# Optimization experiments

Measured on AMD Instinct MI355X. Metric: run time of the kernel, lower is better.

## Reference

```python
import jax, jax.numpy as jnp
import numpy as np

N = 50000      # nodes
E = 800000     # edges (avg degree 16)
IN, HID, OUT = 128, 256, 64
G = 500        # graphs in the batch (100 nodes each)
NEG_SLOPE = 0.01
EPS = 1e-12


def setup_inputs() -> dict:
    key = jax.random.key(0)
    ks = jax.random.split(key, 9)
    x = jax.random.normal(ks[0], (N, IN), jnp.float32)
    edge_index = jax.random.randint(ks[1], (2, E), 0, N, dtype=jnp.int32)
    # sorted segment ids with every graph present (100 nodes per graph)
    batch = jnp.repeat(jnp.arange(G, dtype=jnp.int32), N // G)
    def lin(k, fan_in, fan_out):
        s = 1.0 / np.sqrt(fan_in)
        kw, kb = jax.random.split(k)
        W = jax.random.uniform(kw, (fan_in, fan_out), jnp.float32, -s, s)
        b = jax.random.uniform(kb, (fan_out,), jnp.float32, -s, s)
        return W, b
    W1, b1 = lin(ks[2], IN, HID)
    W2, b2 = lin(ks[3], HID, HID)
    W3, b3 = lin(ks[4], HID, OUT)
    return {"x": x, "edge_index": edge_index, "batch": batch,
            "W1": W1, "b1": b1, "W2": W2, "b2": b2, "W3": W3, "b3": b3}


def _sage_conv(x, edge_index, W, b):
    # SAGEConv(aggr='add', root_weight=False, normalize=True):
    # gather source features, scatter-add to targets, linear, L2 normalize.
    src, dst = edge_index[0], edge_index[1]
    agg = jax.ops.segment_sum(x[src], dst, num_segments=x.shape[0])  # [N, d_in]
    out = agg @ W + b                                                 # [N, d_out]
    nrm = jnp.linalg.norm(out, axis=-1, keepdims=True)
    return out / jnp.maximum(nrm, EPS)


def reference(x, edge_index, batch, W1, b1, W2, b2, W3, b3):
    h = _sage_conv(x, edge_index, W1, b1)
    h = jax.nn.leaky_relu(h, NEG_SLOPE)          # dropout p=0 -> identity
    h = _sage_conv(h, edge_index, W2, b2)
    h = jax.nn.leaky_relu(h, NEG_SLOPE)
    h = _sage_conv(h, edge_index, W3, b3)
    # get_zero_nodes: first node of each graph (batch sorted, all G present)
    mask = jnp.concatenate([jnp.ones((1,), bool), batch[1:] != batch[:-1]])
    first_idx = jnp.nonzero(mask, size=G)[0]
    return h[first_idx]                          # [G, OUT]
```

## Files before the change

### kernel.cpp

```cpp
#include <hip/hip_runtime.h>

#define N_NODES 50000
#define E_EDGES 800000
#define IN_DIM  128
#define HID_DIM 256
#define OUT_DIM 64
#define G_GRAPHS 500
#define CAP 64

typedef __attribute__((ext_vector_type(8))) short short8;
typedef __attribute__((ext_vector_type(4))) float float4v;

__device__ __forceinline__ float bf2f(unsigned short u) {
  union { unsigned int i; float f; } c; c.i = ((unsigned int)u) << 16; return c.f;
}
__device__ __forceinline__ unsigned short f2bf(float f) {
  union { float f; unsigned int i; } c; c.f = f;
  unsigned int x = c.i;
  x += 0x7FFFu + ((x >> 16) & 1u);
  return (unsigned short)(x >> 16);
}
__device__ __forceinline__ unsigned int fbits(float f) {
  union { float f; unsigned int i; } c; c.f = f; return c.i;
}
__device__ __forceinline__ float bits2f(unsigned int u) {
  union { unsigned int i; float f; } c; c.i = u; return c.f;
}


__global__ __launch_bounds__(256) void prep_build(
    const int* __restrict__ src, const int* __restrict__ dst,
    const int* __restrict__ batch,
    const float* __restrict__ x,
    const float* __restrict__ W1, const float* __restrict__ W2,
    int* __restrict__ deg, int* __restrict__ srcs, int* __restrict__ first_node,
    unsigned short* __restrict__ xb,
    unsigned short* __restrict__ W1t, unsigned short* __restrict__ W2t) {
  const int b = blockIdx.x, tid = threadIdx.x;
  if (b < 6250) {
    const int t = b * 256 + tid;
    const int i = t * 4;
    const float4 v = *(const float4*)(x + i);
    ushort4 u;
    u.x = f2bf(v.x); u.y = f2bf(v.y); u.z = f2bf(v.z); u.w = f2bf(v.w);
    *(ushort4*)(xb + i) = u;
    if (t < E_EDGES) {
      const int d = dst[t];
      const int pos = atomicAdd(&deg[d], 1);
      if (pos < CAP) srcs[(d << 6) + pos] = src[t];
    }
    if (t < N_NODES) {
      if (t == 0 || batch[t] != batch[t - 1]) first_node[batch[t]] = t;
    }
  } else {
    const int t = (b - 6250) * 256 + tid;
    if (t < 8192) {
      const int n = t >> 5, k0 = (t & 31) * 4;
      ushort4 o;
      o.x = f2bf(W1[(k0 + 0) * 256 + n]);
      o.y = f2bf(W1[(k0 + 1) * 256 + n]);
      o.z = f2bf(W1[(k0 + 2) * 256 + n]);
      o.w = f2bf(W1[(k0 + 3) * 256 + n]);
      *(ushort4*)&W1t[n * 128 + k0] = o;
    } else {
      const int v2 = t - 8192;
      const int n = v2 >> 6, k0 = (v2 & 63) * 4;
      ushort4 o;
      o.x = f2bf(W2[(k0 + 0) * 256 + n]);
      o.y = f2bf(W2[(k0 + 1) * 256 + n]);
      o.z = f2bf(W2[(k0 + 2) * 256 + n]);
      o.w = f2bf(W2[(k0 + 3) * 256 + n]);
      *(ushort4*)&W2t[n * 256 + k0] = o;
    }
  }
}


__global__ __launch_bounds__(64) void build_list2(
    const int* __restrict__ deg, const int* __restrict__ srcs,
    const int* __restrict__ first_node,
    unsigned char* __restrict__ need1, int* __restrict__ list2,
    int* __restrict__ cnt2) {
  const int g = blockIdx.x;
  const int lane = threadIdx.x;
  const int node = first_node[g];
  const int cnt = min(deg[node], CAP);
  int s = 0;
  if (lane < cnt) s = srcs[(node << 6) + lane];
  const unsigned long long m = __ballot(lane < cnt);
  int base = 0;
  if (lane == 0) base = atomicAdd(cnt2, __popcll(m));
  base = __shfl(base, 0);
  if (lane < cnt) {
    list2[base + lane] = s;
    const int c2 = min(deg[s], CAP);
    for (int q = 0; q < c2; ++q) need1[srcs[(s << 6) + q]] = 1;
  }
}

__global__ __launch_bounds__(256) void compact_list1(
    const unsigned char* __restrict__ need1,
    int* __restrict__ list1, int* __restrict__ cnt1) {
  __shared__ int wbase[4];
  const int tid = threadIdx.x;
  const int lane = tid & 63;
  const int wv = tid >> 6;
  const int i = blockIdx.x * 256 + tid;
  const bool f = (i < N_NODES) && need1[i];
  const unsigned long long m = __ballot(f);
  if (lane == 0) wbase[wv] = __popcll(m);
  __syncthreads();
  if (tid == 0) {
    const int t0 = wbase[0], t1 = wbase[1], t2 = wbase[2], t3 = wbase[3];
    const int b = atomicAdd(cnt1, t0 + t1 + t2 + t3);
    wbase[0] = b; wbase[1] = b + t0; wbase[2] = b + t0 + t1; wbase[3] = b + t0 + t1 + t2;
  }
  __syncthreads();
  if (f) list1[wbase[wv] + __popcll(m & ((1ull << lane) - 1ull))] = i;
}


template<int K>
__global__ __launch_bounds__(512, 8) void fused_layer(
    const unsigned short* __restrict__ H,
    const int* __restrict__ deg, const int* __restrict__ srcs,
    const unsigned short* __restrict__ Wt,
    const float* __restrict__ bias,
    unsigned short* __restrict__ Hout,
    const int* __restrict__ nodelist,
    const int* __restrict__ pcount)
{
  constexpr int M = 256;
  constexpr int TN = 16;
  constexpr int VPT = K / 64;
  constexpr int LDK = K + 8;
  __shared__ unsigned short a_hi[TN][LDK];
  __shared__ unsigned short a_lo[TN][LDK];
  __shared__ float ssq_tot[TN];
  __shared__ int nid_s[TN];
  const int tid = threadIdx.x;
  const int lane = tid & 63;
  const int wv = tid >> 6;

  const int total = __builtin_amdgcn_readfirstlane(*pcount);
  if (blockIdx.x * TN >= total) return;

  if (tid < TN) {
    int gi = blockIdx.x * TN + tid;
    if (gi >= total) gi = total - 1;
    nid_s[tid] = nodelist[gi];
    ssq_tot[tid] = 0.f;
  }
  __syncthreads();

  const unsigned short* hb = H + lane * VPT;
  const int node0 = __builtin_amdgcn_readfirstlane(nid_s[2 * wv]);
  const int node1 = __builtin_amdgcn_readfirstlane(nid_s[2 * wv + 1]);
  const int cnt0 = __builtin_amdgcn_readfirstlane(min(deg[node0], CAP));
  const int cnt1 = __builtin_amdgcn_readfirstlane(min(deg[node1], CAP));
  int idx0 = 0, idx1 = 0;
  if (lane < cnt0) idx0 = srcs[(node0 << 6) + lane];
  if (lane < cnt1) idx1 = srcs[(node1 << 6) + lane];

#pragma unroll
  for (int i = 0; i < 2; ++i) {
    const int nn = 2 * wv + i;
    const int cnt = i ? cnt1 : cnt0;
    const int idx = i ? idx1 : idx0;

    float acc[VPT];
#pragma unroll
    for (int j = 0; j < VPT; ++j) acc[j] = 0.f;

    int j = 0;
    for (; j + 16 <= cnt; j += 16) {
      int s[16];
#pragma unroll
      for (int u = 0; u < 16; ++u) s[u] = __builtin_amdgcn_readlane(idx, j + u);
      if constexpr (VPT == 4) {
        ushort4 r[16];
#pragma unroll
        for (int u = 0; u < 16; ++u) r[u] = *(const ushort4*)(hb + s[u] * K);
#pragma unroll
        for (int u = 0; u < 16; ++u) {
          acc[0] += bf2f(r[u].x); acc[1] += bf2f(r[u].y);
          acc[2] += bf2f(r[u].z); acc[3] += bf2f(r[u].w);
        }
      } else {
        ushort2 r[16];
#pragma unroll
        for (int u = 0; u < 16; ++u) r[u] = *(const ushort2*)(hb + s[u] * K);
#pragma unroll
        for (int u = 0; u < 16; ++u) {
          acc[0] += bf2f(r[u].x); acc[1] += bf2f(r[u].y);
        }
      }
    }
    for (; j < cnt; j += 8) {
      int s[8]; float w[8];
#pragma unroll
      for (int u = 0; u < 8; ++u) {
        const int q = j + u;
        const int qm = (q < cnt) ? q : (cnt - 1);
        s[u] = __builtin_amdgcn_readlane(idx, qm);
        w[u] = (q < cnt) ? 1.f : 0.f;
      }
      if constexpr (VPT == 4) {
        ushort4 r[8];
#pragma unroll
        for (int u = 0; u < 8; ++u) r[u] = *(const ushort4*)(hb + s[u] * K);
#pragma unroll
        for (int u = 0; u < 8; ++u) {
          acc[0] = fmaf(w[u], bf2f(r[u].x), acc[0]);
          acc[1] = fmaf(w[u], bf2f(r[u].y), acc[1]);
          acc[2] = fmaf(w[u], bf2f(r[u].z), acc[2]);
          acc[3] = fmaf(w[u], bf2f(r[u].w), acc[3]);
        }
      } else {
        ushort2 r[8];
#pragma unroll
        for (int u = 0; u < 8; ++u) r[u] = *(const ushort2*)(hb + s[u] * K);
#pragma unroll
        for (int u = 0; u < 8; ++u) {
          acc[0] = fmaf(w[u], bf2f(r[u].x), acc[0]);
          acc[1] = fmaf(w[u], bf2f(r[u].y), acc[1]);
        }
      }
    }

    unsigned short h[VPT], l[VPT];
#pragma unroll
    for (int jj = 0; jj < VPT; ++jj) {
      const unsigned int u = fbits(acc[jj]);
      h[jj] = (unsigned short)(u >> 16);
      const float res = acc[jj] - bits2f(u & 0xFFFF0000u);
      l[jj] = (unsigned short)(fbits(res) >> 16);
    }
    if constexpr (VPT == 4) {
      *(ushort4*)&a_hi[nn][lane * 4] = make_ushort4(h[0], h[1], h[2], h[3]);
      *(ushort4*)&a_lo[nn][lane * 4] = make_ushort4(l[0], l[1], l[2], l[3]);
    } else {
      *(ushort2*)&a_hi[nn][lane * 2] = make_ushort2(h[0], h[1]);
      *(ushort2*)&a_lo[nn][lane * 2] = make_ushort2(l[0], l[1]);
    }
  }
  __syncthreads();

  const int g = lane >> 4;
  const int lc = lane & 15;
  float4v dacc0 = (float4v){0.f, 0.f, 0.f, 0.f};
  float4v dacc1 = (float4v){0.f, 0.f, 0.f, 0.f};
  const unsigned short* W0 = Wt + (size_t)(wv * 16 + lc) * K + g * 8;
  const unsigned short* W1r = Wt + (size_t)((wv + 8) * 16 + lc) * K + g * 8;
#pragma unroll
  for (int ks = 0; ks < K / 32; ++ks) {
    const short8 ah = *(const short8*)&a_hi[lc][ks * 32 + g * 8];
    const short8 al = *(const short8*)&a_lo[lc][ks * 32 + g * 8];
    const short8 b0 = *(const short8*)(W0 + ks * 32);
    const short8 b1 = *(const short8*)(W1r + ks * 32);
    dacc0 = __builtin_amdgcn_mfma_f32_16x16x32_bf16(ah, b0, dacc0, 0, 0, 0);
    dacc0 = __builtin_amdgcn_mfma_f32_16x16x32_bf16(al, b0, dacc0, 0, 0, 0);
    dacc1 = __builtin_amdgcn_mfma_f32_16x16x32_bf16(ah, b1, dacc1, 0, 0, 0);
    dacc1 = __builtin_amdgcn_mfma_f32_16x16x32_bf16(al, b1, dacc1, 0, 0, 0);
  }

  const float bn0 = bias[wv * 16 + lc];
  const float bn1 = bias[(wv + 8) * 16 + lc];
  float4v o0 = dacc0 + bn0;
  float4v o1 = dacc1 + bn1;
  float sq[4];
#pragma unroll
  for (int r = 0; r < 4; ++r) sq[r] = o0[r] * o0[r] + o1[r] * o1[r];
#pragma unroll
  for (int off = 1; off < 16; off <<= 1) {
#pragma unroll
    for (int r = 0; r < 4; ++r) sq[r] += __shfl_xor(sq[r], off);
  }
  if (lc == 0) {
#pragma unroll
    for (int r = 0; r < 4; ++r) atomicAdd(&ssq_tot[g * 4 + r], sq[r]);
  }
  __syncthreads();

#pragma unroll
  for (int r = 0; r < 4; ++r) {
    const float inv = 1.f / fmaxf(sqrtf(ssq_tot[g * 4 + r]), 1e-12f);
    float v0 = o0[r] * inv;
    float v1 = o1[r] * inv;
    v0 = (v0 >= 0.f) ? v0 : 0.01f * v0;
    v1 = (v1 >= 0.f) ? v1 : 0.01f * v1;
    const int nd = nid_s[g * 4 + r];
    Hout[(size_t)nd * M + wv * 16 + lc] = f2bf(v0);
    Hout[(size_t)nd * M + (wv + 8) * 16 + lc] = f2bf(v1);
  }
}


__global__ __launch_bounds__(64) void layer3_kernel(
    const unsigned short* __restrict__ H2,
    const int* __restrict__ deg, const int* __restrict__ srcs,
    const int* __restrict__ first_node,
    const float* __restrict__ W,
    const float* __restrict__ bias,
    float* __restrict__ out)
{
  __shared__ float a_s[HID_DIM];
  const int g = blockIdx.x;
  const int lane = threadIdx.x;
  const int node = first_node[g];
  const int cnt = min(deg[node], CAP);
  float acc[4] = {0.f, 0.f, 0.f, 0.f};
  for (int p = 0; p < cnt; ++p) {
    const int s = srcs[(node << 6) + p];
    const ushort4 u = *(const ushort4*)(H2 + (size_t)s * HID_DIM + lane * 4);
    acc[0] += bf2f(u.x); acc[1] += bf2f(u.y); acc[2] += bf2f(u.z); acc[3] += bf2f(u.w);
  }
  *(float4*)&a_s[lane * 4] = make_float4(acc[0], acc[1], acc[2], acc[3]);
  __syncthreads();
  float o = bias[lane];
#pragma unroll 8
  for (int k = 0; k < HID_DIM; ++k) o += a_s[k] * W[k * OUT_DIM + lane];
  float ss = o * o;
#pragma unroll
  for (int off = 32; off > 0; off >>= 1) ss += __shfl_xor(ss, off);
  const float inv = 1.f / fmaxf(sqrtf(ss), 1e-12f);
  out[(size_t)g * OUT_DIM + lane] = o * inv;
}


extern "C" void kernel_launch(void* const* d_in, const int* in_sizes, int n_in,
                              void* d_out, int out_size, void* d_ws, size_t ws_size,
                              hipStream_t stream) {
  (void)in_sizes; (void)n_in; (void)out_size; (void)ws_size;
  const float* x   = (const float*)d_in[0];
  const int* ei    = (const int*)d_in[1];
  const int* batch = (const int*)d_in[2];
  const float* W1  = (const float*)d_in[3];
  const float* b1  = (const float*)d_in[4];
  const float* W2  = (const float*)d_in[5];
  const float* b2  = (const float*)d_in[6];
  const float* W3  = (const float*)d_in[7];
  const float* b3  = (const float*)d_in[8];
  const int* src = ei;
  const int* dst = ei + E_EDGES;

  char* ws = (char*)d_ws;
  size_t off = 0;
  auto alloc = [&](size_t bytes) {
    void* p = ws + off;
    off = (off + bytes + 255) & ~(size_t)255;
    return p;
  };
  int* deg    = (int*)alloc((size_t)N_NODES * 4);
  unsigned char* need1 = (unsigned char*)alloc((size_t)N_NODES);
  int* cnts   = (int*)alloc(256);
  const size_t zero_len = off;
  int* cnt1 = cnts;
  int* cnt2 = cnts + 1;

  int* srcs   = (int*)alloc((size_t)N_NODES * CAP * 4);
  int* first  = (int*)alloc((size_t)G_GRAPHS * 4);
  int* list1  = (int*)alloc((size_t)N_NODES * 4);
  int* list2  = (int*)alloc((size_t)G_GRAPHS * CAP * 4);
  unsigned short* W1t = (unsigned short*)alloc((size_t)256 * 128 * 2);
  unsigned short* W2t = (unsigned short*)alloc((size_t)256 * 256 * 2);
  unsigned short* h2 = (unsigned short*)alloc((size_t)N_NODES * HID_DIM * 2);
  unsigned short* xb = h2;
  unsigned short* h1 = (unsigned short*)alloc((size_t)N_NODES * HID_DIM * 2);

  hipMemsetAsync(deg, 0, zero_len, stream);

  prep_build<<<6346, 256, 0, stream>>>(src, dst, batch, x, W1, W2,
                                       deg, srcs, first, xb, W1t, W2t);

  build_list2<<<G_GRAPHS, 64, 0, stream>>>(deg, srcs, first, need1, list2, cnt2);
  compact_list1<<<(N_NODES + 255) / 256, 256, 0, stream>>>(need1, list1, cnt1);

  fused_layer<IN_DIM><<<N_NODES / 16, 512, 0, stream>>>(xb, deg, srcs, W1t, b1, h1,
                                                        list1, cnt1);
  fused_layer<HID_DIM><<<(G_GRAPHS * CAP) / 16, 512, 0, stream>>>(h1, deg, srcs, W2t, b2, h2,
                                                                  list2, cnt2);
  layer3_kernel<<<G_GRAPHS, 64, 0, stream>>>(h2, deg, srcs, first, W3, b3, (float*)d_out);
}
```

Measured before the change: 228.4 us.

## Build adjacency via two-pass binned scatter with 16-bit source ids

Replaces the per-edge global atomic insertion into the capped adjacency list with a two-pass scheme. Edges are first bucketed by destination bin using shared-memory counters, then each bin builds its nodes' neighbor lists in shared memory and writes them out contiguously. Source ids are stored as 16-bit values, which halves the adjacency footprint and read traffic in later kernels. This adds an extra kernel launch and an intermediate bin buffer whose fixed capacity could silently drop edges on skewed inputs.

```diff
diff --git a/kernel.cpp b/kernel.cpp
--- a/kernel.cpp
+++ b/kernel.cpp
@@ -7,6 +7,8 @@
 #define OUT_DIM 64
 #define G_GRAPHS 500
 #define CAP 64
+#define NBINS 196
+#define BINCAP 5120
 
 typedef __attribute__((ext_vector_type(8))) short short8;
 typedef __attribute__((ext_vector_type(4))) float float4v;
@@ -28,32 +30,60 @@
 }
 
 
-__global__ __launch_bounds__(256) void prep_build(
+__global__ __launch_bounds__(256) void prep1(
     const int* __restrict__ src, const int* __restrict__ dst,
     const int* __restrict__ batch,
     const float* __restrict__ x,
     const float* __restrict__ W1, const float* __restrict__ W2,
-    int* __restrict__ deg, int* __restrict__ srcs, int* __restrict__ first_node,
+    unsigned int* __restrict__ binbuf, int* __restrict__ bin_next,
+    int* __restrict__ first_node,
     unsigned short* __restrict__ xb,
     unsigned short* __restrict__ W1t, unsigned short* __restrict__ W2t) {
   const int b = blockIdx.x, tid = threadIdx.x;
-  if (b < 6250) {
-    const int t = b * 256 + tid;
+  if (b < 200) {
+    __shared__ int cnt[NBINS];
+    __shared__ int gbase[NBINS];
+    for (int i = tid; i < NBINS; i += 256) cnt[i] = 0;
+    __syncthreads();
+    const int base = b * 4096;
+    unsigned int pk[16]; int bp[16];
+#pragma unroll
+    for (int u = 0; u < 16; ++u) {
+      const int e = base + u * 256 + tid;
+      bp[u] = -1;
+      if (e < E_EDGES) {
+        const int d = dst[e];
+        const int s = src[e];
+        const int bin = d >> 8;
+        const int pos = atomicAdd(&cnt[bin], 1);
+        pk[u] = ((unsigned int)(d & 255) << 16) | (unsigned int)s;
+        bp[u] = (bin << 16) | pos;
+      }
+    }
+    __syncthreads();
+    for (int i = tid; i < NBINS; i += 256)
+      gbase[i] = atomicAdd(&bin_next[i], cnt[i]);
+    __syncthreads();
+#pragma unroll
+    for (int u = 0; u < 16; ++u) {
+      if (bp[u] >= 0) {
+        const int bin = bp[u] >> 16, pos = bp[u] & 0xFFFF;
+        const int idx = gbase[bin] + pos;
+        if (idx < BINCAP) binbuf[bin * BINCAP + idx] = pk[u];
+      }
+    }
+  } else if (b < 6450) {
+    const int t = (b - 200) * 256 + tid;
     const int i = t * 4;
     const float4 v = *(const float4*)(x + i);
     ushort4 u;
     u.x = f2bf(v.x); u.y = f2bf(v.y); u.z = f2bf(v.z); u.w = f2bf(v.w);
     *(ushort4*)(xb + i) = u;
-    if (t < E_EDGES) {
-      const int d = dst[t];
-      const int pos = atomicAdd(&deg[d], 1);
-      if (pos < CAP) srcs[(d << 6) + pos] = src[t];
-    }
     if (t < N_NODES) {
       if (t == 0 || batch[t] != batch[t - 1]) first_node[batch[t]] = t;
     }
   } else {
-    const int t = (b - 6250) * 256 + tid;
+    const int t = (b - 6450) * 256 + tid;
     if (t < 8192) {
       const int n = t >> 5, k0 = (t & 31) * 4;
       ushort4 o;
@@ -76,8 +106,36 @@
 }
 
 
+__global__ __launch_bounds__(512) void prep2(
+    const unsigned int* __restrict__ binbuf, const int* __restrict__ bin_next,
+    int* __restrict__ deg, unsigned short* __restrict__ srcs) {
+  __shared__ unsigned short img[256 * CAP];
+  __shared__ int cnt[256];
+  const int tid = threadIdx.x;
+  const int bin = blockIdx.x;
+  if (tid < 256) cnt[tid] = 0;
+  __syncthreads();
+  const int total = min(bin_next[bin], BINCAP);
+  const unsigned int* bb = binbuf + bin * BINCAP;
+  for (int i = tid; i < total; i += 512) {
+    const unsigned int pk = bb[i];
+    const int nl = pk >> 16;
+    const int pos = atomicAdd(&cnt[nl], 1);
+    if (pos < CAP) img[(nl << 6) + pos] = (unsigned short)(pk & 0xFFFFu);
+  }
+  __syncthreads();
+  const int node0 = bin << 8;
+  const int nend = min(N_NODES, node0 + 256);
+  if (tid < 256 && node0 + tid < nend) deg[node0 + tid] = cnt[tid];
+  const int nwords = (nend - node0) * 32;
+  unsigned int* dstw = (unsigned int*)(srcs + ((size_t)node0 << 6));
+  const unsigned int* srcw = (const unsigned int*)img;
+  for (int i = tid; i < nwords; i += 512) dstw[i] = srcw[i];
+}
+
+
 __global__ __launch_bounds__(64) void build_list2(
-    const int* __restrict__ deg, const int* __restrict__ srcs,
+    const int* __restrict__ deg, const unsigned short* __restrict__ srcs,
     const int* __restrict__ first_node,
     unsigned char* __restrict__ need1, int* __restrict__ list2,
     int* __restrict__ cnt2) {
@@ -123,7 +181,7 @@
 template<int K>
 __global__ __launch_bounds__(512, 8) void fused_layer(
     const unsigned short* __restrict__ H,
-    const int* __restrict__ deg, const int* __restrict__ srcs,
+    const int* __restrict__ deg, const unsigned short* __restrict__ srcs,
     const unsigned short* __restrict__ Wt,
     const float* __restrict__ bias,
     unsigned short* __restrict__ Hout,
@@ -298,7 +356,7 @@
 
 __global__ __launch_bounds__(64) void layer3_kernel(
     const unsigned short* __restrict__ H2,
-    const int* __restrict__ deg, const int* __restrict__ srcs,
+    const int* __restrict__ deg, const unsigned short* __restrict__ srcs,
     const int* __restrict__ first_node,
     const float* __restrict__ W,
     const float* __restrict__ bias,
@@ -351,27 +409,30 @@
     off = (off + bytes + 255) & ~(size_t)255;
     return p;
   };
-  int* deg    = (int*)alloc((size_t)N_NODES * 4);
   unsigned char* need1 = (unsigned char*)alloc((size_t)N_NODES);
-  int* cnts   = (int*)alloc(256);
+  int* cnts    = (int*)alloc(256);
+  int* bin_next= (int*)alloc((size_t)NBINS * 4);
   const size_t zero_len = off;
   int* cnt1 = cnts;
   int* cnt2 = cnts + 1;
 
-  int* srcs   = (int*)alloc((size_t)N_NODES * CAP * 4);
+  int* deg    = (int*)alloc((size_t)N_NODES * 4);
+  unsigned short* srcs = (unsigned short*)alloc((size_t)N_NODES * CAP * 2);
   int* first  = (int*)alloc((size_t)G_GRAPHS * 4);
   int* list1  = (int*)alloc((size_t)N_NODES * 4);
   int* list2  = (int*)alloc((size_t)G_GRAPHS * CAP * 4);
+  unsigned int* binbuf = (unsigned int*)alloc((size_t)NBINS * BINCAP * 4);
   unsigned short* W1t = (unsigned short*)alloc((size_t)256 * 128 * 2);
   unsigned short* W2t = (unsigned short*)alloc((size_t)256 * 256 * 2);
   unsigned short* h2 = (unsigned short*)alloc((size_t)N_NODES * HID_DIM * 2);
   unsigned short* xb = h2;
   unsigned short* h1 = (unsigned short*)alloc((size_t)N_NODES * HID_DIM * 2);
 
-  hipMemsetAsync(deg, 0, zero_len, stream);
-
-  prep_build<<<6346, 256, 0, stream>>>(src, dst, batch, x, W1, W2,
-                                       deg, srcs, first, xb, W1t, W2t);
+  hipMemsetAsync(need1, 0, zero_len, stream);
+
+  prep1<<<6546, 256, 0, stream>>>(src, dst, batch, x, W1, W2,
+                                  binbuf, bin_next, first, xb, W1t, W2t);
+  prep2<<<NBINS, 512, 0, stream>>>(binbuf, bin_next, deg, srcs);
 
   build_list2<<<G_GRAPHS, 64, 0, stream>>>(deg, srcs, first, need1, list2, cnt2);
   compact_list1<<<(N_NODES + 255) / 256, 256, 0, stream>>>(need1, list1, cnt1);
```

After: 202.5 us. 1.13x faster.
